# Kernel tuning notes

Measured on AMD Instinct MI355X. Metric: run time of the kernel, lower is better.

The kernel has to match this reference:

```python
import jax, jax.numpy as jnp
import numpy as np

EMBED_DIM = 512
NUM_HEADS = 8
TGT_LEN = 1024
BSZ = 16


def setup_inputs() -> dict:
    key = jax.random.key(0)
    ks = jax.random.split(key, 6)
    E = EMBED_DIM
    query = jax.random.normal(ks[0], (TGT_LEN, BSZ, E), jnp.float32)
    i_proj = jax.random.normal(ks[1], (3 * E,), jnp.float32)
    # xavier_uniform-ish scale for (3E, E)
    lim = (6.0 / (3 * E + E)) ** 0.5
    in_proj_weight = jax.random.uniform(ks[2], (3 * E, E), jnp.float32, -lim, lim)
    in_proj_bias = jnp.zeros((3 * E,), jnp.float32)
    lim2 = (6.0 / (2 * E)) ** 0.5
    out_w = jax.random.uniform(ks[3], (E, E), jnp.float32, -lim2, lim2)
    out_b = jnp.zeros((E,), jnp.float32)
    bias_k = jax.random.normal(ks[4], (1, 1, E), jnp.float32)
    bias_v = jax.random.normal(ks[5], (1, 1, E), jnp.float32)
    return dict(query=query, i_proj=i_proj, in_proj_weight=in_proj_weight,
                in_proj_bias=in_proj_bias, out_w=out_w, out_b=out_b,
                bias_k=bias_k, bias_v=bias_v)


def reference(query, i_proj, in_proj_weight, in_proj_bias, out_w, out_b, bias_k, bias_v):
    # qkv_same path: key = value = query (self-attention)
    T, B, E = query.shape
    H = NUM_HEADS
    hd = E // H
    scaling = hd ** -0.5
    # per-call weight mutation: every 3rd column replaced by i_proj
    w = in_proj_weight.at[:, ::3].set(i_proj[:, None])
    qkv = jnp.einsum('tbe,fe->tbf', query, w) + in_proj_bias  # (T, B, 3E)
    q, k, v = jnp.split(qkv, 3, axis=-1)
    q = q * scaling
    k = jnp.concatenate([k, jnp.broadcast_to(bias_k, (1, B, E))], axis=0)  # (T+1, B, E)
    v = jnp.concatenate([v, jnp.broadcast_to(bias_v, (1, B, E))], axis=0)
    S = k.shape[0]
    q = q.reshape(T, B * H, hd).transpose(1, 0, 2)  # (B*H, T, hd)
    k = k.reshape(S, B * H, hd).transpose(1, 0, 2)  # (B*H, S, hd)
    v = v.reshape(S, B * H, hd).transpose(1, 0, 2)
    aw = jnp.einsum('nth,nsh->nts', q, k)  # (B*H, T, S)
    # global min-max normalization over the entire score tensor (not softmax)
    mn = jnp.min(aw)
    mx = jnp.max(aw)
    aw = (aw - mn) / (mx - mn)
    attn = jnp.einsum('nts,nsh->nth', aw, v)  # (B*H, T, hd)
    attn = attn.transpose(1, 0, 2).reshape(T, B, E)
    attn = attn @ out_w.T + out_b  # out_proj
    aw_avg = aw.reshape(B, H, T, S).sum(axis=1) / H  # (B, T, S)
    wq, wk, wv = jnp.split(w, 3, axis=0)
    w_ret = jnp.stack([wq.T, wk.T, wv.T], axis=0)  # (3, E, E)
    return attn, aw_avg, w_ret
```

## Files before the change

kernel.cpp:

```cpp
#include <hip/hip_runtime.h>
#include <hip/hip_bf16.h>
#include <stdint.h>

typedef __bf16 bf16;
typedef __bf16 bf16x8 __attribute__((ext_vector_type(8)));
typedef __bf16 bf16x4 __attribute__((ext_vector_type(4)));
typedef float  f32x4  __attribute__((ext_vector_type(4)));

#define MFMA_BF16(a,b,c) __builtin_amdgcn_mfma_f32_16x16x32_bf16((a),(b),(c),0,0,0)

#define WS_QBF_IN  0L
#define WS_WBF     16777216L
#define WS_OUTWBF  18350080L
#define WS_Q       18874368L
#define WS_K       35651584L
#define WS_V       52428800L
#define WS_VT      69206016L
#define WS_AWLAST  85983232L
#define WS_VCS     86507520L
#define WS_MM      86540288L
#define WS_KT      86540544L
#define WS_KTV     103317760L

__device__ __forceinline__ void gload16(const void* g, void* l) {
  __builtin_amdgcn_global_load_lds((const __attribute__((address_space(1))) uint32_t*)g,
                                   (__attribute__((address_space(3))) uint32_t*)l, 16, 0, 0);
}
__device__ __forceinline__ unsigned ordf(float x) {
  unsigned b = __float_as_uint(x);
  return (b & 0x80000000u) ? ~b : (b | 0x80000000u);
}
__device__ __forceinline__ float deordf(unsigned u) {
  unsigned b = (u & 0x80000000u) ? (u ^ 0x80000000u) : ~u;
  return __uint_as_float(b);
}

__global__ __launch_bounds__(256) void cvt_query_kernel(const float* __restrict__ in,
                                                        bf16* __restrict__ out) {
  long i = (long)blockIdx.x * 256 + threadIdx.x;
  for (; i < 2097152L; i += (long)gridDim.x * 256) {
    float4 v = ((const float4*)in)[i];
    bf16x4 o; o[0] = (bf16)v.x; o[1] = (bf16)v.y; o[2] = (bf16)v.z; o[3] = (bf16)v.w;
    ((bf16x4*)out)[i] = o;
  }
}

__global__ __launch_bounds__(256) void prep_weights_kernel(
    const float* __restrict__ in_w, const float* __restrict__ i_proj,
    const float* __restrict__ out_w, bf16* __restrict__ w_bf,
    bf16* __restrict__ outw_bf, float* __restrict__ w_ret,
    unsigned* __restrict__ mm) {
  long idx = (long)blockIdx.x * 256 + threadIdx.x;
  if (idx == 0) { mm[0] = 0xFFFFFFFFu; mm[1] = 0u; }
  if (idx < 786432L) {
    int f = (int)(idx >> 9), e = (int)(idx & 511);
    float val = (e % 3 == 0) ? i_proj[f] : in_w[idx];
    w_bf[idx] = (bf16)val;
    w_ret[(long)(f >> 9) * 262144 + (long)e * 512 + (f & 511)] = val;
  } else if (idx < 1048576L) {
    long j = idx - 786432L;
    outw_bf[j] = (bf16)out_w[j];
  }
}

template <int MODE>
__global__ __launch_bounds__(256, 2) void gemm_kernel(
    const bf16* __restrict__ A, const bf16* __restrict__ B,
    const float* __restrict__ bias,
    bf16* __restrict__ q_out, bf16* __restrict__ k_out, bf16* __restrict__ v_out,
    float* __restrict__ outC) {
  const int K = 512;
  __shared__ __align__(16) bf16 aTile[128 * 32];
  __shared__ __align__(16) bf16 bTile[128 * 32];
  const int tid = threadIdx.x;
  const int lane = tid & 63, w = tid >> 6;
  const int l15 = lane & 15, l4 = lane >> 4;
  const long r0 = (long)blockIdx.y * 128;
  const long f0 = (long)blockIdx.x * 128;
  const int rm = (w >> 1) * 64, cn = (w & 1) * 64;
  const int srow = tid >> 2;
  const int scc = tid & 3;
  f32x4 acc[4][4] = {};

  for (int kk = 0; kk < K; kk += 32) {
#pragma unroll
    for (int i = 0; i < 2; ++i) {
      int row = srow + i * 64;
      int cc = scc ^ (row & 3);
      gload16(A + (r0 + row) * K + kk + cc * 8, (char*)aTile + (w * 64 + i * 256) * 16);
    }
#pragma unroll
    for (int i = 0; i < 2; ++i) {
      int row = srow + i * 64;
      int cc = scc ^ (row & 3);
      gload16(B + (f0 + row) * K + kk + cc * 8, (char*)bTile + (w * 64 + i * 256) * 16);
    }
    __syncthreads();
    bf16x8 af[4], bfr[4];
#pragma unroll
    for (int mi = 0; mi < 4; ++mi) {
      int r = rm + mi * 16 + l15;
      int c = l4 ^ (r & 3);
      af[mi] = *(const bf16x8*)((const char*)aTile + r * 64 + c * 16);
    }
#pragma unroll
    for (int ni = 0; ni < 4; ++ni) {
      int r = cn + ni * 16 + l15;
      int c = l4 ^ (r & 3);
      bfr[ni] = *(const bf16x8*)((const char*)bTile + r * 64 + c * 16);
    }
#pragma unroll
    for (int mi = 0; mi < 4; ++mi)
#pragma unroll
      for (int ni = 0; ni < 4; ++ni)
        acc[mi][ni] = MFMA_BF16(af[mi], bfr[ni], acc[mi][ni]);
    __syncthreads();
  }
#pragma unroll
  for (int mi = 0; mi < 4; ++mi)
#pragma unroll
    for (int ni = 0; ni < 4; ++ni)
#pragma unroll
      for (int r = 0; r < 4; ++r) {
        long row = r0 + rm + mi * 16 + l4 * 4 + r;
        int f = (int)f0 + cn + ni * 16 + l15;
        float val = acc[mi][ni][r] + bias[f];
        if (MODE == 0) {
          int t = (int)(row >> 4), b = (int)(row & 15);
          int which = f >> 9, hh = (f >> 6) & 7, d = f & 63;
          long off = ((long)(b * 8 + hh) * 1024 + t) * 64 + d;
          if (which == 0)      q_out[off] = (bf16)(val * 0.125f);
          else if (which == 1) k_out[off] = (bf16)val;
          else                 v_out[off] = (bf16)val;
        } else {
          outC[row * 512 + f] = val;
        }
      }
}

#define AWS_STAGE(h_, buf_)                                                        \
  do {                                                                             \
    _Pragma("unroll")                                                              \
    for (int i_ = 0; i_ < 4; ++i_) {                                               \
      int row_ = i_ * 32 + wrow;                                                   \
      gload16(q_bf + ((long)(b * 8 + (h_)) * 1024 + t0 + row_) * 64 + scc8 * 8,    \
              (char*)aT[buf_] + (i_ * 256 + w * 64) * 16);                         \
      gload16(k_bf + ((long)(b * 8 + (h_)) * 1024 + s0 + row_) * 64 + scc8 * 8,    \
              (char*)bT[buf_] + (i_ * 256 + w * 64) * 16);                         \
    }                                                                              \
  } while (0)

#define AWS_COMPUTE(buf_)                                                          \
  do {                                                                             \
    _Pragma("unroll")                                                              \
    for (int ks_ = 0; ks_ < 2; ++ks_) {                                            \
      bf16x8 af[4], bfr[4];                                                        \
      _Pragma("unroll")                                                            \
      for (int mi_ = 0; mi_ < 4; ++mi_) {                                          \
        int r_ = rm + mi_ * 16 + l15;                                              \
        int p_ = (ks_ * 4 + l4) ^ (r_ & 7);                                        \
        af[mi_] = *(const bf16x8*)((const char*)aT[buf_] + r_ * 128 + p_ * 16);    \
      }                                                                            \
      _Pragma("unroll")                                                            \
      for (int ni_ = 0; ni_ < 4; ++ni_) {                                          \
        int r_ = cn + ni_ * 16 + l15;                                              \
        int p_ = (ks_ * 4 + l4) ^ (r_ & 7);                                        \
        bfr[ni_] = *(const bf16x8*)((const char*)bT[buf_] + r_ * 128 + p_ * 16);   \
      }                                                                            \
      _Pragma("unroll")                                                            \
      for (int mi_ = 0; mi_ < 4; ++mi_)                                            \
        _Pragma("unroll")                                                          \
        for (int ni_ = 0; ni_ < 4; ++ni_)                                          \
          acc[mi_][ni_] = MFMA_BF16(af[mi_], bfr[ni_], acc[mi_][ni_]);             \
    }                                                                              \
  } while (0)

__global__ __launch_bounds__(256, 2) void awsum_gemm_kernel(
    const bf16* __restrict__ q_bf, const bf16* __restrict__ k_bf,
    bf16* __restrict__ aw_raw, unsigned* __restrict__ mm) {
  __shared__ __align__(16) bf16 aT[2][128 * 64];
  __shared__ __align__(16) bf16 bT[2][128 * 64];
  const int tid = threadIdx.x;
  const int lane = tid & 63, w = tid >> 6;
  const int l15 = lane & 15, l4 = lane >> 4;
  const int bid = blockIdx.x;
  const int xcd = bid & 7, slot = bid >> 3;
  const int b = xcd * 2 + (slot >> 6);
  const int rest = slot & 63;
  const int t0 = (rest >> 3) * 128;
  const int s0 = (rest & 7) * 128;
  const int rm = (w >> 1) * 64, cn = (w & 1) * 64;
  const int wrow = w * 8 + (lane >> 3);
  const int scc8 = (lane & 7) ^ ((lane >> 3) & 7);

  f32x4 acc[4][4] = {};
  f32x4 snap[4][4] = {};
  float vmin = 1e30f, vmax = -1e30f;

  AWS_STAGE(0, 0);
  AWS_STAGE(1, 1);
  asm volatile("s_waitcnt vmcnt(8)" ::: "memory");
  __builtin_amdgcn_s_barrier();
  __builtin_amdgcn_sched_barrier(0);
#pragma unroll
  for (int h = 0; h < 8; ++h) {
    AWS_COMPUTE(h & 1);
#pragma unroll
    for (int mi = 0; mi < 4; ++mi)
#pragma unroll
      for (int ni = 0; ni < 4; ++ni) {
        f32x4 d = acc[mi][ni] - snap[mi][ni];
#pragma unroll
        for (int r = 0; r < 4; ++r) {
          vmin = fminf(vmin, d[r]);
          vmax = fmaxf(vmax, d[r]);
        }
        snap[mi][ni] = acc[mi][ni];
      }
    __builtin_amdgcn_s_barrier();
    __builtin_amdgcn_sched_barrier(0);
    if (h + 2 < 8) AWS_STAGE(h + 2, h & 1);
    if (h + 1 < 8) {
      if (h + 2 < 8) asm volatile("s_waitcnt vmcnt(8)" ::: "memory");
      else           asm volatile("s_waitcnt vmcnt(0)" ::: "memory");
      __builtin_amdgcn_s_barrier();
      __builtin_amdgcn_sched_barrier(0);
    }
  }
#pragma unroll
  for (int mi = 0; mi < 4; ++mi)
#pragma unroll
    for (int ni = 0; ni < 4; ++ni)
#pragma unroll
      for (int r = 0; r < 4; ++r) {
        int t = t0 + rm + mi * 16 + l4 * 4 + r;
        int s = s0 + cn + ni * 16 + l15;
        aw_raw[((long)b * 1024 + t) * 1024 + s] = (bf16)acc[mi][ni][r];
      }
#pragma unroll
  for (int off = 32; off; off >>= 1) {
    vmin = fminf(vmin, __shfl_xor(vmin, off));
    vmax = fmaxf(vmax, __shfl_xor(vmax, off));
  }
  if (lane == 0) { atomicMin(&mm[0], ordf(vmin)); atomicMax(&mm[1], ordf(vmax)); }
}

__global__ __launch_bounds__(256) void transpose_kv_kernel(
    const bf16* __restrict__ k_bf, const bf16* __restrict__ v_bf,
    bf16* __restrict__ kT, bf16* __restrict__ vT) {
  const bf16* src = blockIdx.z ? v_bf : k_bf;
  bf16* dst = blockIdx.z ? vT : kT;
  const int n = blockIdx.y;
  const long s0 = (long)blockIdx.x * 64;
  __shared__ __align__(16) bf16 tile[64][72];
  const int tid = threadIdx.x;
  const int row = tid >> 3, cc = tid & 7;
#pragma unroll
  for (int it = 0; it < 2; ++it) {
    int r = row + it * 32;
    bf16x8 vv = *(const bf16x8*)(src + ((long)n * 1024 + s0 + r) * 64 + cc * 8);
    *(bf16x8*)&tile[r][cc * 8] = vv;
  }
  __syncthreads();
#pragma unroll
  for (int it = 0; it < 2; ++it) {
    int d = row + it * 32;
    bf16x8 ov;
#pragma unroll
    for (int j = 0; j < 8; ++j) ov[j] = tile[cc * 8 + j][d];
    *(bf16x8*)(dst + ((long)n * 64 + d) * 1024 + s0 + cc * 8) = ov;
  }
}

__global__ __launch_bounds__(256) void vcolsum_kernel(const bf16* __restrict__ vT,
                                                      const float* __restrict__ bias_v,
                                                      float* __restrict__ vcs) {
  const int n = blockIdx.x, h = n & 7;
  const int d = threadIdx.x >> 2, q = threadIdx.x & 3;
  float acc = 0.f;
  const bf16* row = vT + (long)n * 65536 + (long)d * 1024 + q * 256;
#pragma unroll 4
  for (int j = 0; j < 32; ++j) {
    bf16x8 v = *(const bf16x8*)(row + j * 8);
#pragma unroll
    for (int e = 0; e < 8; ++e) acc += (float)v[e];
  }
  __shared__ float red[256];
  red[threadIdx.x] = acc;
  __syncthreads();
  if (q == 0)
    vcs[n * 64 + d] = red[d * 4] + red[d * 4 + 1] + red[d * 4 + 2] + red[d * 4 + 3] +
                      bias_v[h * 64 + d];
}

__global__ __launch_bounds__(256) void ktv_kernel(const bf16* __restrict__ kT,
                                                  const bf16* __restrict__ vT,
                                                  bf16* __restrict__ ktvT) {
  const int n = blockIdx.x;
  const int tid = threadIdx.x;
  const int lane = tid & 63, w = tid >> 6;
  const int l15 = lane & 15, l4 = lane >> 4;
  const int wr = w >> 1, wc = w & 1;
  f32x4 acc[2][2] = {};
  const bf16* kbase = kT + (long)n * 65536;
  const bf16* vbase = vT + (long)n * 65536;
  for (int s0 = 0; s0 < 1024; s0 += 32) {
    bf16x8 af[2], bfr[2];
#pragma unroll
    for (int mi = 0; mi < 2; ++mi)
      af[mi] = *(const bf16x8*)(kbase + (long)(wr * 32 + mi * 16 + l15) * 1024 + s0 + l4 * 8);
#pragma unroll
    for (int ni = 0; ni < 2; ++ni)
      bfr[ni] = *(const bf16x8*)(vbase + (long)(wc * 32 + ni * 16 + l15) * 1024 + s0 + l4 * 8);
#pragma unroll
    for (int mi = 0; mi < 2; ++mi)
#pragma unroll
      for (int ni = 0; ni < 2; ++ni)
        acc[mi][ni] = MFMA_BF16(af[mi], bfr[ni], acc[mi][ni]);
  }
#pragma unroll
  for (int mi = 0; mi < 2; ++mi)
#pragma unroll
    for (int ni = 0; ni < 2; ++ni)
#pragma unroll
      for (int r = 0; r < 4; ++r) {
        int d = wr * 32 + mi * 16 + l4 * 4 + r;
        int dp = wc * 32 + ni * 16 + l15;
        ktvT[(long)n * 4096 + dp * 64 + d] = (bf16)acc[mi][ni][r];
      }
}

__global__ __launch_bounds__(256) void qattn_kernel(
    const bf16* __restrict__ q_bf, const bf16* __restrict__ ktvT,
    const float* __restrict__ aw_last, const float* __restrict__ vcs,
    const float* __restrict__ bias_v, const unsigned* __restrict__ mm,
    bf16* __restrict__ A2) {
  const int tid = threadIdx.x;
  const int lane = tid & 63, w = tid >> 6;
  const int l15 = lane & 15, l4 = lane >> 4;
  const int t0 = blockIdx.x * 64;
  const int h = blockIdx.y * 4 + w;
  const int b = blockIdx.z;
  const long n = (long)b * 8 + h;
  f32x4 acc[4][4] = {};
  const bf16* qbase = q_bf + (n * 1024 + t0) * 64;
  const bf16* kbase = ktvT + (long)n * 4096;
#pragma unroll
  for (int kk = 0; kk < 64; kk += 32) {
    bf16x8 af[4], bfr[4];
#pragma unroll
    for (int mi = 0; mi < 4; ++mi)
      af[mi] = *(const bf16x8*)(qbase + (mi * 16 + l15) * 64 + kk + l4 * 8);
#pragma unroll
    for (int ni = 0; ni < 4; ++ni)
      bfr[ni] = *(const bf16x8*)(kbase + (ni * 16 + l15) * 64 + kk + l4 * 8);
#pragma unroll
    for (int mi = 0; mi < 4; ++mi)
#pragma unroll
      for (int ni = 0; ni < 4; ++ni)
        acc[mi][ni] = MFMA_BF16(af[mi], bfr[ni], acc[mi][ni]);
  }
  float mn = deordf(mm[0]), mx = deordf(mm[1]);
  float a = 1.f / (mx - mn), c = -mn * a;
#pragma unroll
  for (int mi = 0; mi < 4; ++mi)
#pragma unroll
    for (int r = 0; r < 4; ++r) {
      int t = t0 + mi * 16 + l4 * 4 + r;
      float alast = a * aw_last[n * 1024 + t];
#pragma unroll
      for (int ni = 0; ni < 4; ++ni) {
        int dp = ni * 16 + l15;
        float val = a * acc[mi][ni][r] + alast * bias_v[h * 64 + dp] + c * vcs[n * 64 + dp];
        A2[((long)t * 16 + b) * 512 + h * 64 + dp] = (bf16)val;
      }
    }
}

__global__ __launch_bounds__(256) void bias_col_kernel(const bf16* __restrict__ q_bf,
                                                       const float* __restrict__ bias_k,
                                                       float* __restrict__ aw_last,
                                                       unsigned* __restrict__ mm) {
  const int n = blockIdx.y, h = n & 7;
  const int t = blockIdx.x * 256 + threadIdx.x;
  float acc = 0.f;
  const bf16* qrow = q_bf + ((long)n * 1024 + t) * 64;
#pragma unroll
  for (int j = 0; j < 8; ++j) {
    bf16x8 qv = *(const bf16x8*)(qrow + j * 8);
#pragma unroll
    for (int e = 0; e < 8; ++e) acc += (float)qv[e] * bias_k[h * 64 + j * 8 + e];
  }
  aw_last[(long)n * 1024 + t] = acc;
  float vmin = acc, vmax = acc;
#pragma unroll
  for (int off = 32; off; off >>= 1) {
    vmin = fminf(vmin, __shfl_xor(vmin, off));
    vmax = fmaxf(vmax, __shfl_xor(vmax, off));
  }
  if ((threadIdx.x & 63) == 0) { atomicMin(&mm[0], ordf(vmin)); atomicMax(&mm[1], ordf(vmax)); }
}

__global__ __launch_bounds__(256) void rescale_kernel(const bf16* __restrict__ aw_raw,
                                                      float* __restrict__ aw_out,
                                                      const float* __restrict__ aw_last,
                                                      const unsigned* __restrict__ mm) {
  long idx = (long)blockIdx.x * 256 + threadIdx.x;
  float mn = deordf(mm[0]), mx = deordf(mm[1]);
  float a = 1.f / (mx - mn), c = -mn * a;
  int s = (int)(idx % 1025);
  long bt = idx / 1025;
  float v;
  if (s < 1024) {
    v = (float)aw_raw[bt * 1024 + s];
  } else {
    int b = (int)(bt >> 10), t = (int)(bt & 1023);
    v = 0.f;
#pragma unroll
    for (int h = 0; h < 8; ++h) v += aw_last[(long)(b * 8 + h) * 1024 + t];
  }
  aw_out[idx] = fmaf(a, v * 0.125f, c);
}

extern "C" void kernel_launch(void* const* d_in, const int* in_sizes, int n_in,
                              void* d_out, int out_size, void* d_ws, size_t ws_size,
                              hipStream_t stream) {
  const float* query  = (const float*)d_in[0];
  const float* i_proj = (const float*)d_in[1];
  const float* in_w   = (const float*)d_in[2];
  const float* in_b   = (const float*)d_in[3];
  const float* out_w  = (const float*)d_in[4];
  const float* out_b  = (const float*)d_in[5];
  const float* bias_k = (const float*)d_in[6];
  const float* bias_v = (const float*)d_in[7];
  float* out = (float*)d_out;

  char* ws = (char*)d_ws;
  bf16* qbf_in = (bf16*)(ws + WS_QBF_IN);
  bf16* w_bf   = (bf16*)(ws + WS_WBF);
  bf16* outwbf = (bf16*)(ws + WS_OUTWBF);
  bf16* q_bf   = (bf16*)(ws + WS_Q);
  bf16* k_bf   = (bf16*)(ws + WS_K);
  bf16* v_bf   = (bf16*)(ws + WS_V);
  bf16* vT     = (bf16*)(ws + WS_VT);
  bf16* kT     = (bf16*)(ws + WS_KT);
  bf16* ktvT   = (bf16*)(ws + WS_KTV);
  bf16* aw_raw = (bf16*)(ws + WS_V);
  float* aw_last = (float*)(ws + WS_AWLAST);
  float* vcs     = (float*)(ws + WS_VCS);
  unsigned* mm   = (unsigned*)(ws + WS_MM);
  bf16* A2 = qbf_in;

  float* out_attn  = out;
  float* out_awavg = out + 8388608L;
  float* out_wret  = out + 25182208L;

  cvt_query_kernel<<<2048, 256, 0, stream>>>(query, qbf_in);
  prep_weights_kernel<<<4096, 256, 0, stream>>>(in_w, i_proj, out_w, w_bf, outwbf, out_wret, mm);
  gemm_kernel<0><<<dim3(12, 128), 256, 0, stream>>>(qbf_in, w_bf, in_b, q_bf, k_bf, v_bf, nullptr);
  transpose_kv_kernel<<<dim3(16, 128, 2), 256, 0, stream>>>(k_bf, v_bf, kT, vT);
  vcolsum_kernel<<<128, 256, 0, stream>>>(vT, bias_v, vcs);
  bias_col_kernel<<<dim3(4, 128), 256, 0, stream>>>(q_bf, bias_k, aw_last, mm);
  ktv_kernel<<<128, 256, 0, stream>>>(kT, vT, ktvT);
  awsum_gemm_kernel<<<1024, 256, 0, stream>>>(q_bf, k_bf, aw_raw, mm);
  rescale_kernel<<<65600, 256, 0, stream>>>(aw_raw, out_awavg, aw_last, mm);
  qattn_kernel<<<dim3(16, 2, 16), 256, 0, stream>>>(q_bf, ktvT, aw_last, vcs, bias_v, mm, A2);
  gemm_kernel<1><<<dim3(4, 128), 256, 0, stream>>>(A2, outwbf, out_b, nullptr, nullptr, nullptr, out_attn);
}
```

Measured before the change: 311.8 us.

## Double-buffer projection GEMM with 64-wide K tiles and async staging

Rewrites the QKV and output projection GEMM to match the awsum kernel's pipeline: K tiles of 64 held in two LDS buffers, with the next stage's global-to-LDS loads issued while the current tile is computed, synchronised through vmcnt waits and raw barriers. The aim is to hide global load latency and halve the number of barrier round trips per K loop. Both kernels now share the compute macro and use the same swizzled staging index scheme. LDS use per block rises to 64KB, which may limit occupancy below the declared two blocks per SM.

After: 306.7 us. Within noise of the previous version (-1.6%).

```diff
diff --git a/kernel.cpp b/kernel.cpp
--- a/kernel.cpp
+++ b/kernel.cpp
@@ -63,94 +63,21 @@
   }
 }
 
-template <int MODE>
-__global__ __launch_bounds__(256, 2) void gemm_kernel(
-    const bf16* __restrict__ A, const bf16* __restrict__ B,
-    const float* __restrict__ bias,
-    bf16* __restrict__ q_out, bf16* __restrict__ k_out, bf16* __restrict__ v_out,
-    float* __restrict__ outC) {
-  const int K = 512;
-  __shared__ __align__(16) bf16 aTile[128 * 32];
-  __shared__ __align__(16) bf16 bTile[128 * 32];
-  const int tid = threadIdx.x;
-  const int lane = tid & 63, w = tid >> 6;
-  const int l15 = lane & 15, l4 = lane >> 4;
-  const long r0 = (long)blockIdx.y * 128;
-  const long f0 = (long)blockIdx.x * 128;
-  const int rm = (w >> 1) * 64, cn = (w & 1) * 64;
-  const int srow = tid >> 2;
-  const int scc = tid & 3;
-  f32x4 acc[4][4] = {};
-
-  for (int kk = 0; kk < K; kk += 32) {
-#pragma unroll
-    for (int i = 0; i < 2; ++i) {
-      int row = srow + i * 64;
-      int cc = scc ^ (row & 3);
-      gload16(A + (r0 + row) * K + kk + cc * 8, (char*)aTile + (w * 64 + i * 256) * 16);
-    }
-#pragma unroll
-    for (int i = 0; i < 2; ++i) {
-      int row = srow + i * 64;
-      int cc = scc ^ (row & 3);
-      gload16(B + (f0 + row) * K + kk + cc * 8, (char*)bTile + (w * 64 + i * 256) * 16);
-    }
-    __syncthreads();
-    bf16x8 af[4], bfr[4];
-#pragma unroll
-    for (int mi = 0; mi < 4; ++mi) {
-      int r = rm + mi * 16 + l15;
-      int c = l4 ^ (r & 3);
-      af[mi] = *(const bf16x8*)((const char*)aTile + r * 64 + c * 16);
-    }
-#pragma unroll
-    for (int ni = 0; ni < 4; ++ni) {
-      int r = cn + ni * 16 + l15;
-      int c = l4 ^ (r & 3);
-      bfr[ni] = *(const bf16x8*)((const char*)bTile + r * 64 + c * 16);
-    }
-#pragma unroll
-    for (int mi = 0; mi < 4; ++mi)
-#pragma unroll
-      for (int ni = 0; ni < 4; ++ni)
-        acc[mi][ni] = MFMA_BF16(af[mi], bfr[ni], acc[mi][ni]);
-    __syncthreads();
-  }
-#pragma unroll
-  for (int mi = 0; mi < 4; ++mi)
-#pragma unroll
-    for (int ni = 0; ni < 4; ++ni)
-#pragma unroll
-      for (int r = 0; r < 4; ++r) {
-        long row = r0 + rm + mi * 16 + l4 * 4 + r;
-        int f = (int)f0 + cn + ni * 16 + l15;
-        float val = acc[mi][ni][r] + bias[f];
-        if (MODE == 0) {
-          int t = (int)(row >> 4), b = (int)(row & 15);
-          int which = f >> 9, hh = (f >> 6) & 7, d = f & 63;
-          long off = ((long)(b * 8 + hh) * 1024 + t) * 64 + d;
-          if (which == 0)      q_out[off] = (bf16)(val * 0.125f);
-          else if (which == 1) k_out[off] = (bf16)val;
-          else                 v_out[off] = (bf16)val;
-        } else {
-          outC[row * 512 + f] = val;
-        }
-      }
-}
-
-#define AWS_STAGE(h_, buf_)                                                        \
+#define PIPE_STAGE(Abase_, Bbase_, kk_, buf_)                                      \
   do {                                                                             \
     _Pragma("unroll")                                                              \
     for (int i_ = 0; i_ < 4; ++i_) {                                               \
-      int row_ = i_ * 32 + wrow;                                                   \
-      gload16(q_bf + ((long)(b * 8 + (h_)) * 1024 + t0 + row_) * 64 + scc8 * 8,    \
+      int c_ = tid + i_ * 256;                                                     \
+      int row_ = c_ >> 3;                                                          \
+      int cc_ = (c_ & 7) ^ (row_ & 7);                                             \
+      gload16((Abase_) + (long)row_ * 512 + (kk_) + cc_ * 8,                       \
               (char*)aT[buf_] + (i_ * 256 + w * 64) * 16);                         \
-      gload16(k_bf + ((long)(b * 8 + (h_)) * 1024 + s0 + row_) * 64 + scc8 * 8,    \
+      gload16((Bbase_) + (long)row_ * 512 + (kk_) + cc_ * 8,                       \
               (char*)bT[buf_] + (i_ * 256 + w * 64) * 16);                         \
     }                                                                              \
   } while (0)
 
-#define AWS_COMPUTE(buf_)                                                          \
+#define PIPE_COMPUTE(buf_)                                                         \
   do {                                                                             \
     _Pragma("unroll")                                                              \
     for (int ks_ = 0; ks_ < 2; ++ks_) {                                            \
@@ -175,6 +102,64 @@
     }                                                                              \
   } while (0)
 
+template <int MODE>
+__global__ __launch_bounds__(256, 2) void gemm_kernel(
+    const bf16* __restrict__ A, const bf16* __restrict__ B,
+    const float* __restrict__ bias,
+    bf16* __restrict__ q_out, bf16* __restrict__ k_out, bf16* __restrict__ v_out,
+    float* __restrict__ outC) {
+  __shared__ __align__(16) bf16 aT[2][128 * 64];
+  __shared__ __align__(16) bf16 bT[2][128 * 64];
+  const int tid = threadIdx.x;
+  const int lane = tid & 63, w = tid >> 6;
+  const int l15 = lane & 15, l4 = lane >> 4;
+  const long r0 = (long)blockIdx.y * 128;
+  const long f0 = (long)blockIdx.x * 128;
+  const int rm = (w >> 1) * 64, cn = (w & 1) * 64;
+  const bf16* Ab = A + r0 * 512;
+  const bf16* Bb = B + f0 * 512;
+  f32x4 acc[4][4] = {};
+
+  PIPE_STAGE(Ab, Bb, 0, 0);
+  PIPE_STAGE(Ab, Bb, 64, 1);
+  asm volatile("s_waitcnt vmcnt(8)" ::: "memory");
+  __builtin_amdgcn_s_barrier();
+  __builtin_amdgcn_sched_barrier(0);
+#pragma unroll
+  for (int k = 0; k < 8; ++k) {
+    PIPE_COMPUTE(k & 1);
+    __builtin_amdgcn_s_barrier();
+    __builtin_amdgcn_sched_barrier(0);
+    if (k + 2 < 8) PIPE_STAGE(Ab, Bb, (k + 2) * 64, k & 1);
+    if (k + 1 < 8) {
+      if (k + 2 < 8) asm volatile("s_waitcnt vmcnt(8)" ::: "memory");
+      else           asm volatile("s_waitcnt vmcnt(0)" ::: "memory");
+      __builtin_amdgcn_s_barrier();
+      __builtin_amdgcn_sched_barrier(0);
+    }
+  }
+#pragma unroll
+  for (int mi = 0; mi < 4; ++mi)
+#pragma unroll
+    for (int ni = 0; ni < 4; ++ni)
+#pragma unroll
+      for (int r = 0; r < 4; ++r) {
+        long row = r0 + rm + mi * 16 + l4 * 4 + r;
+        int f = (int)f0 + cn + ni * 16 + l15;
+        float val = acc[mi][ni][r] + bias[f];
+        if (MODE == 0) {
+          int t = (int)(row >> 4), b = (int)(row & 15);
+          int which = f >> 9, hh = (f >> 6) & 7, d = f & 63;
+          long off = ((long)(b * 8 + hh) * 1024 + t) * 64 + d;
+          if (which == 0)      q_out[off] = (bf16)(val * 0.125f);
+          else if (which == 1) k_out[off] = (bf16)val;
+          else                 v_out[off] = (bf16)val;
+        } else {
+          outC[row * 512 + f] = val;
+        }
+      }
+}
+
 __global__ __launch_bounds__(256, 2) void awsum_gemm_kernel(
     const bf16* __restrict__ q_bf, const bf16* __restrict__ k_bf,
     bf16* __restrict__ aw_raw, unsigned* __restrict__ mm) {
@@ -190,21 +175,35 @@
   const int t0 = (rest >> 3) * 128;
   const int s0 = (rest & 7) * 128;
   const int rm = (w >> 1) * 64, cn = (w & 1) * 64;
-  const int wrow = w * 8 + (lane >> 3);
-  const int scc8 = (lane & 7) ^ ((lane >> 3) & 7);
+  const bf16* qb = q_bf + (long)b * 8 * 65536 + (long)t0 * 64;
+  const bf16* kb = k_bf + (long)b * 8 * 65536 + (long)s0 * 64;
 
   f32x4 acc[4][4] = {};
   f32x4 snap[4][4] = {};
   float vmin = 1e30f, vmax = -1e30f;
 
-  AWS_STAGE(0, 0);
-  AWS_STAGE(1, 1);
+#define AWS_STAGE13(h_, buf_)                                                      \
+  do {                                                                             \
+    _Pragma("unroll")                                                              \
+    for (int i_ = 0; i_ < 4; ++i_) {                                               \
+      int c_ = tid + i_ * 256;                                                     \
+      int row_ = c_ >> 3;                                                          \
+      int cc_ = (c_ & 7) ^ (row_ & 7);                                             \
+      gload16(qb + (long)(h_) * 65536 + (long)row_ * 64 + cc_ * 8,                 \
+              (char*)aT[buf_] + (i_ * 256 + w * 64) * 16);                         \
+      gload16(kb + (long)(h_) * 65536 + (long)row_ * 64 + cc_ * 8,                 \
+              (char*)bT[buf_] + (i_ * 256 + w * 64) * 16);                         \
+    }                                                                              \
+  } while (0)
+
+  AWS_STAGE13(0, 0);
+  AWS_STAGE13(1, 1);
   asm volatile("s_waitcnt vmcnt(8)" ::: "memory");
   __builtin_amdgcn_s_barrier();
   __builtin_amdgcn_sched_barrier(0);
 #pragma unroll
   for (int h = 0; h < 8; ++h) {
-    AWS_COMPUTE(h & 1);
+    PIPE_COMPUTE(h & 1);
 #pragma unroll
     for (int mi = 0; mi < 4; ++mi)
 #pragma unroll
@@ -219,7 +218,7 @@
       }
     __builtin_amdgcn_s_barrier();
     __builtin_amdgcn_sched_barrier(0);
-    if (h + 2 < 8) AWS_STAGE(h + 2, h & 1);
+    if (h + 2 < 8) AWS_STAGE13(h + 2, h & 1);
     if (h + 1 < 8) {
       if (h + 2 < 8) asm volatile("s_waitcnt vmcnt(8)" ::: "memory");
       else           asm volatile("s_waitcnt vmcnt(0)" ::: "memory");
```
